# Performance work log

Hardware: AMD Instinct MI355X
Metric: run time of the kernel (lower is better)

## Reference

```python
import jax, jax.numpy as jnp
import numpy as np
import math

DIM = 256
PATCH = 16  # Patchnum
H = W = 64  # feature_size
B = 16


def _conv(x, w, pad):
    # x: [B,C,H,W], w: [O,I,kh,kw]
    return jax.lax.conv_general_dilated(
        x, w, window_strides=(1, 1), padding=[(pad, pad), (pad, pad)],
        dimension_numbers=('NCHW', 'OIHW', 'NCHW'))


def setup_inputs() -> dict:
    key = jax.random.key(0)
    ks = jax.random.split(key, 6)
    fan = DIM * 9
    s3 = 1.0 / math.sqrt(fan)
    s1 = 1.0 / math.sqrt(DIM)
    return {
        'e': jax.random.normal(ks[0], (B, DIM, H, W), dtype=jnp.float32),
        'pam_out': jax.random.normal(ks[1], (B, DIM, PATCH, PATCH), dtype=jnp.float32),
        'q_w': jax.random.uniform(ks[2], (DIM, DIM, 3, 3), jnp.float32, -s3, s3),
        'k_w': jax.random.uniform(ks[3], (DIM, DIM, 3, 3), jnp.float32, -s3, s3),
        'v_w': jax.random.uniform(ks[4], (DIM, DIM, 3, 3), jnp.float32, -s3, s3),
        'proj_w': jax.random.uniform(ks[5], (DIM, DIM, 1, 1), jnp.float32, -s1, s1),
    }


def reference(e, pam_out, q_w, k_w, v_w, proj_w):
    b, c, h, w = e.shape
    # AdaptiveAvgPool2d((PATCH, PATCH)) with h % PATCH == 0 -> mean pooling
    fh, fw = h // PATCH, w // PATCH
    max_e = e.reshape(b, c, PATCH, fh, PATCH, fw).mean(axis=(3, 5))
    q = _conv(max_e, q_w, 1).reshape(b, c, PATCH * PATCH)      # [b,c,P^2]
    k = _conv(pam_out, k_w, 1).reshape(b, c, PATCH * PATCH)    # [b,c,P^2]
    v = _conv(e, v_w, 1).reshape(b, c, h * w)                  # [b,c,HW]
    # L2 normalize along token dim (torch F.normalize, eps=1e-12)
    q = q / jnp.maximum(jnp.linalg.norm(q, axis=-1, keepdims=True), 1e-12)
    k = k / jnp.maximum(jnp.linalg.norm(k, axis=-1, keepdims=True), 1e-12)
    attn = jnp.einsum('bcn,bdn->bcd', q, k) / math.sqrt(c)     # [b,c,c]
    attn = jax.nn.softmax(attn, axis=-1)
    out = jnp.einsum('bcd,bdn->bcn', attn, v).reshape(b, c, h, w)
    out = _conv(out, proj_w, 0) + e
    return out
```

## Files before the change

### kernel.cpp

```cpp
#include <hip/hip_runtime.h>
#include <hip/hip_bf16.h>

#define NB 16
#define NC 256
#define NPIX 4096

typedef __attribute__((ext_vector_type(8))) short short8;
typedef __attribute__((ext_vector_type(4))) short short4v;
typedef __attribute__((ext_vector_type(4))) float f32x4;

static __device__ __forceinline__ ushort f2bf(float f) {
    __hip_bfloat16 h = __float2bfloat16(f);
    return *(ushort*)&h;
}

static __device__ __forceinline__ void gload_lds16(const ushort* g, ushort* l) {
    __builtin_amdgcn_global_load_lds(
        (const __attribute__((address_space(1))) unsigned int*)g,
        (__attribute__((address_space(3))) unsigned int*)l, 16, 0, 0);
}

__global__ void __launch_bounds__(256) prep_k(
    const float* __restrict__ e, const float* __restrict__ pam,
    const float* __restrict__ qw, const float* __restrict__ kw,
    const float* __restrict__ vw, const float* __restrict__ pw,
    ushort* __restrict__ et, ushort* __restrict__ maxeT, ushort* __restrict__ pamT,
    ushort* __restrict__ wqT, ushort* __restrict__ wkT,
    ushort* __restrict__ pbf, ushort* __restrict__ vwT,
    float* __restrict__ qnorm, float* __restrict__ knorm) {
    __shared__ float smem[9216];
    int blk = blockIdx.x, t = threadIdx.x;
    if (blk < 512) {
        int b = blk >> 5;
        int py = (blk >> 1) & 15;
        int xh = blk & 1;
        float (*lt)[32] = (float(*)[32])smem;
        float pool[8];
#pragma unroll
        for (int rr = 0; rr < 8; ++rr) pool[rr] = 0.f;
        int px = t & 7;
        int x4 = px * 4;
        int cg = t >> 3;
        for (int r = 0; r < 4; ++r) {
            int y = py * 4 + r;
            if (r) __syncthreads();
            const float* ep = e + (size_t)b * NC * NPIX + y * 64 + xh * 32;
#pragma unroll
            for (int rr = 0; rr < 8; ++rr) {
                int c = rr * 32 + cg;
                float4 v = *(const float4*)(ep + (size_t)c * NPIX + x4);
                pool[rr] += v.x + v.y + v.z + v.w;
                int s = (c >> 3) & 31;
                lt[c][(x4 + 0) ^ s] = v.x;
                lt[c][(x4 + 1) ^ s] = v.y;
                lt[c][(x4 + 2) ^ s] = v.z;
                lt[c][(x4 + 3) ^ s] = v.w;
            }
            __syncthreads();
            int l = t & 31, c0 = l * 8;
            ushort* op = et + ((size_t)((b * 64 + y) * 64) + xh * 32) * 256;
#pragma unroll
            for (int rx = 0; rx < 4; ++rx) {
                int x = rx * 8 + (t >> 5);
                short8 v;
#pragma unroll
                for (int k = 0; k < 8; ++k) v[k] = (short)f2bf(lt[c0 + k][x ^ l]);
                *(short8*)(op + (size_t)x * 256 + c0) = v;
            }
        }
        int tok = py * 16 + xh * 8 + px;
        ushort* md = maxeT + (size_t)b * 65536 + (size_t)tok * 256;
#pragma unroll
        for (int rr = 0; rr < 8; ++rr)
            md[rr * 32 + cg] = f2bf(pool[rr] * 0.0625f);
    } else if (blk < 768) {
        int bb = blk - 512;
        int b = bb >> 4, cg = bb & 15;
        float (*lt)[256] = (float(*)[256])smem;
#pragma unroll
        for (int cc = 0; cc < 16; ++cc)
            lt[cc][t] = pam[(size_t)(b * 256 + cg * 16 + cc) * 256 + t];
        __syncthreads();
        ushort* dstb = pamT + (size_t)b * 65536 + (size_t)t * 256 + cg * 16;
#pragma unroll
        for (int g = 0; g < 2; ++g) {
            short8 v;
#pragma unroll
            for (int k = 0; k < 8; ++k) v[k] = (short)f2bf(lt[g * 8 + k][t]);
            *(short8*)(dstb + g * 8) = v;
        }
    } else if (blk < 1280) {
        int idx = blk - 768;
        const float* src = (idx < 256) ? qw : kw;
        ushort* dst = (idx < 256) ? wqT : wkT;
        int o = idx & 255;
        float wv[9];
#pragma unroll
        for (int j = 0; j < 9; ++j) wv[j] = src[(size_t)o * 2304 + t * 9 + j];
#pragma unroll
        for (int j = 0; j < 9; ++j) dst[(size_t)j * 65536 + (size_t)o * 256 + t] = f2bf(wv[j]);
    } else if (blk < 1296) {
        int base = (blk - 1280) * 4096;
        for (int g = 0; g < 16; ++g) {
            int idx = base + g * 256 + t;
            pbf[idx] = f2bf(pw[idx]);
        }
    } else if (blk < 1360) {
        int d0 = (blk - 1296) * 4;
        float* lt = smem;
        for (int u = 0; u < 36; ++u) lt[u * 256 + t] = vw[(size_t)d0 * 2304 + u * 256 + t];
        __syncthreads();
#pragma unroll
        for (int r = 0; r < 9; ++r) {
            int idx = r * 256 + t;
            int i = idx / 9, j = idx % 9;
            short4v v;
#pragma unroll
            for (int dd = 0; dd < 4; ++dd) v[dd] = (short)f2bf(lt[dd * 2304 + idx]);
            *(short4v*)(vwT + ((size_t)(j * 256 + i)) * 256 + d0) = v;
        }
    } else {
        for (int g = 0; g < 16; ++g) {
            qnorm[g * 256 + t] = 0.f;
            knorm[g * 256 + t] = 0.f;
        }
    }
}

__global__ void __launch_bounds__(256, 2) conv16_mfma(const ushort* __restrict__ maxeT,
                                                      const ushort* __restrict__ pamT,
                                                      const ushort* __restrict__ wqT,
                                                      const ushort* __restrict__ wkT,
                                                      ushort* __restrict__ qb,
                                                      ushort* __restrict__ kTb,
                                                      float* __restrict__ qnorm,
                                                      float* __restrict__ knorm) {
    int blk = blockIdx.x;
    int qk = blk >> 8;
    int b  = (blk >> 4) & 15;
    int og = (blk >> 2) & 3;
    int tg = blk & 3;
    const ushort* inT = qk ? pamT : maxeT;
    const ushort* wt  = qk ? wkT : wqT;
    ushort* outp      = qk ? kTb : qb;
    float* nrm        = qk ? knorm : qnorm;
    int tid = threadIdx.x, wid = tid >> 6, lane = tid & 63;
    int wm = wid >> 1, wn = wid & 1;
    int kq = lane >> 4, l16 = lane & 15;
    int ty0 = tg * 4;
    __shared__ ushort Bs[96][256];
    __shared__ ushort As[2][64][128];
    const ushort* itb = inT + (size_t)b * 65536;
    {
#pragma unroll
        for (int j = 0; j < 12; ++j) {
            int d = (j * 4 + wid) * 64 + lane;
            int tok = d >> 5, u = d & 31;
            int lr = tok >> 4, tx = tok & 15;
            int gy = min(max(ty0 - 1 + lr, 0), 15);
            gload_lds16(itb + (gy * 16 + tx) * 256 + ((u ^ (tok & 7)) * 8),
                        &Bs[0][0] + (size_t)(j * 4 + wid) * 512);
        }
    }
    int aoff[4];
#pragma unroll
    for (int j = 0; j < 4; ++j) {
        int d = (j * 4 + wid) * 64 + lane;
        int o = d >> 4, u = d & 15;
        aoff[j] = (og * 64 + o) * 256 + ((u ^ (o & 7)) * 8);
    }
    auto stageA = [&](int s, int buf) {
        const ushort* base = wt + (size_t)(s >> 1) * 65536 + (s & 1) * 128;
#pragma unroll
        for (int j = 0; j < 4; ++j)
            gload_lds16(base + aoff[j], &As[buf][0][0] + (size_t)(j * 4 + wid) * 512);
    };
    stageA(0, 0);
    stageA(1, 1);
    __syncthreads();
    f32x4 acc[2][2];
#pragma unroll
    for (int mf = 0; mf < 2; ++mf)
#pragma unroll
        for (int nf = 0; nf < 2; ++nf) acc[mf][nf] = (f32x4){0.f, 0.f, 0.f, 0.f};
    const short8 zf = {};
#pragma unroll
    for (int s = 0; s < 18; ++s) {
        int tap = s >> 1, half = s & 1;
        int dy = tap / 3 - 1, dx = tap % 3 - 1;
        const ushort* bp[2]; bool ok[2]; int lt7[2];
#pragma unroll
        for (int nf = 0; nf < 2; ++nf) {
            int n = tg * 64 + wn * 32 + nf * 16 + l16;
            int ny = (n >> 4) + dy, nx = (n & 15) + dx;
            ok[nf] = ((unsigned)ny < 16u) && ((unsigned)nx < 16u);
            int lrc = min(max(ny - ty0 + 1, 0), 5);
            int nxc = min(max(nx, 0), 15);
            int ltok = lrc * 16 + nxc;
            bp[nf] = &Bs[ltok][0];
            lt7[nf] = ltok & 7;
        }
#pragma unroll
        for (int kc = 0; kc < 4; ++kc) {
            int ua = kc * 4 + kq;
            int ub = half * 16 + kc * 4 + kq;
            short8 af[2], bfr[2];
#pragma unroll
            for (int mf = 0; mf < 2; ++mf) {
                int o = wm * 32 + mf * 16 + l16;
                af[mf] = *(const short8*)(&As[s & 1][o][(ua ^ (o & 7)) * 8]);
            }
#pragma unroll
            for (int nf = 0; nf < 2; ++nf) {
                short8 v = *(const short8*)(bp[nf] + ((ub ^ lt7[nf]) * 8));
                bfr[nf] = ok[nf] ? v : zf;
            }
#pragma unroll
            for (int mf = 0; mf < 2; ++mf)
#pragma unroll
                for (int nf = 0; nf < 2; ++nf)
                    acc[mf][nf] = __builtin_amdgcn_mfma_f32_16x16x32_bf16(af[mf], bfr[nf], acc[mf][nf], 0, 0, 0);
        }
        __syncthreads();
        if (s + 2 < 18) stageA(s + 2, s & 1);
    }
    float ss[2][4];
#pragma unroll
    for (int mf = 0; mf < 2; ++mf)
#pragma unroll
        for (int r = 0; r < 4; ++r) ss[mf][r] = 0.f;
#pragma unroll
    for (int mf = 0; mf < 2; ++mf)
#pragma unroll
        for (int nf = 0; nf < 2; ++nf)
#pragma unroll
            for (int r = 0; r < 4; ++r) ss[mf][r] += acc[mf][nf][r] * acc[mf][nf][r];
#pragma unroll
    for (int mf = 0; mf < 2; ++mf)
#pragma unroll
        for (int r = 0; r < 4; ++r) {
#pragma unroll
            for (int off = 1; off < 16; off <<= 1) ss[mf][r] += __shfl_xor(ss[mf][r], off, 64);
        }
    if (l16 == 0) {
#pragma unroll
        for (int mf = 0; mf < 2; ++mf)
#pragma unroll
            for (int r = 0; r < 4; ++r)
                atomicAdd(&nrm[b * 256 + og * 64 + wm * 32 + mf * 16 + kq * 4 + r], ss[mf][r]);
    }
    ushort* ob = outp + (size_t)b * 65536;
#pragma unroll
    for (int mf = 0; mf < 2; ++mf)
#pragma unroll
        for (int nf = 0; nf < 2; ++nf) {
            int col = tg * 64 + wn * 32 + nf * 16 + l16;
#pragma unroll
            for (int r = 0; r < 4; ++r) {
                int row = og * 64 + wm * 32 + mf * 16 + kq * 4 + r;
                ob[(size_t)row * 256 + col] = f2bf(acc[mf][nf][r]);
            }
        }
}

__global__ void __launch_bounds__(512) attn_mfma(const ushort* __restrict__ qb,
                                                 const ushort* __restrict__ kTb,
                                                 const float* __restrict__ qnorm,
                                                 const float* __restrict__ knorm,
                                                 ushort* __restrict__ attnT) {
    int blk = blockIdx.x;
    int b = (blk & 7) + 8 * ((blk >> 3) & 1);
    int cg = blk >> 4;
    int tid = threadIdx.x, wid = tid >> 6, lane = tid & 63;
    int rw = wid & 1, chf = wid >> 1;
    int kq = lane >> 4, l16 = lane & 15;
    int c0w = cg * 32 + rw * 16;
    int lrow = rw * 16 + kq * 4;
    f32x4 acc[4];
#pragma unroll
    for (int nf = 0; nf < 4; ++nf) acc[nf] = (f32x4){0.f, 0.f, 0.f, 0.f};
    const ushort* qp = qb + (size_t)b * 65536;
    const ushort* kp = kTb + (size_t)b * 65536 + (size_t)(chf * 64) * 256;
    for (int kc = 0; kc < 8; ++kc) {
        short8 af = *(const short8*)(qp + (size_t)(c0w + l16) * 256 + kc * 32 + kq * 8);
#pragma unroll
        for (int nf = 0; nf < 4; ++nf) {
            short8 bf = *(const short8*)(kp + (size_t)(nf * 16 + l16) * 256 + kc * 32 + kq * 8);
            acc[nf] = __builtin_amdgcn_mfma_f32_16x16x32_bf16(af, bf, acc[nf], 0, 0, 0);
        }
    }
    float rq[4], rk[4];
#pragma unroll
    for (int r = 0; r < 4; ++r)
        rq[r] = rsqrtf(fmaxf(qnorm[b * 256 + c0w + kq * 4 + r], 1e-24f)) * 0.0625f;
#pragma unroll
    for (int nf = 0; nf < 4; ++nf)
        rk[nf] = rsqrtf(fmaxf(knorm[b * 256 + chf * 64 + nf * 16 + l16], 1e-24f));
#pragma unroll
    for (int nf = 0; nf < 4; ++nf)
#pragma unroll
        for (int r = 0; r < 4; ++r) acc[nf][r] *= rq[r] * rk[nf];
    __shared__ float red[32][4];
    float m4[4], s4[4];
#pragma unroll
    for (int r = 0; r < 4; ++r) {
        float m = -1e30f;
#pragma unroll
        for (int nf = 0; nf < 4; ++nf) m = fmaxf(m, acc[nf][r]);
#pragma unroll
        for (int off = 1; off < 16; off <<= 1) m = fmaxf(m, __shfl_xor(m, off, 64));
        m4[r] = m;
    }
    if (l16 == 0) {
#pragma unroll
        for (int r = 0; r < 4; ++r) red[lrow + r][chf] = m4[r];
    }
    __syncthreads();
#pragma unroll
    for (int r = 0; r < 4; ++r)
        m4[r] = fmaxf(fmaxf(red[lrow + r][0], red[lrow + r][1]),
                      fmaxf(red[lrow + r][2], red[lrow + r][3]));
    __syncthreads();
#pragma unroll
    for (int r = 0; r < 4; ++r) {
        float s = 0.f;
#pragma unroll
        for (int nf = 0; nf < 4; ++nf) {
            float ex = __expf(acc[nf][r] - m4[r]);
            acc[nf][r] = ex;
            s += ex;
        }
#pragma unroll
        for (int off = 1; off < 16; off <<= 1) s += __shfl_xor(s, off, 64);
        s4[r] = s;
    }
    if (l16 == 0) {
#pragma unroll
        for (int r = 0; r < 4; ++r) red[lrow + r][chf] = s4[r];
    }
    __syncthreads();
#pragma unroll
    for (int r = 0; r < 4; ++r) {
        float inv = 1.0f / (red[lrow + r][0] + red[lrow + r][1] +
                            red[lrow + r][2] + red[lrow + r][3]);
#pragma unroll
        for (int nf = 0; nf < 4; ++nf) acc[nf][r] *= inv;
    }
    ushort* ap = attnT + (size_t)b * 65536;
#pragma unroll
    for (int nf = 0; nf < 4; ++nf) {
        int d = chf * 64 + nf * 16 + l16;
        short4v v;
#pragma unroll
        for (int r = 0; r < 4; ++r) v[r] = (short)f2bf(acc[nf][r]);
        *(short4v*)(ap + (size_t)d * 256 + c0w + kq * 4) = v;
    }
}

__global__ void __launch_bounds__(512) mproj_mfma(const ushort* __restrict__ pbf,
                                                  const ushort* __restrict__ attnT,
                                                  ushort* __restrict__ Mbf) {
    int blk = blockIdx.x;
    int b = (blk & 7) + 8 * ((blk >> 3) & 1);
    int og = blk >> 4;
    int tid = threadIdx.x, wid = tid >> 6, lane = tid & 63;
    int rw = wid & 1, chf = wid >> 1;
    int kq = lane >> 4, l16 = lane & 15;
    int o0w = og * 32 + rw * 16;
    f32x4 acc[4];
#pragma unroll
    for (int nf = 0; nf < 4; ++nf) acc[nf] = (f32x4){0.f, 0.f, 0.f, 0.f};
    const ushort* ap = attnT + (size_t)b * 65536 + (size_t)(chf * 64) * 256;
    for (int kc = 0; kc < 8; ++kc) {
        short8 af = *(const short8*)(pbf + (size_t)(o0w + l16) * 256 + kc * 32 + kq * 8);
#pragma unroll
        for (int nf = 0; nf < 4; ++nf) {
            short8 bf = *(const short8*)(ap + (size_t)(nf * 16 + l16) * 256 + kc * 32 + kq * 8);
            acc[nf] = __builtin_amdgcn_mfma_f32_16x16x32_bf16(af, bf, acc[nf], 0, 0, 0);
        }
    }
    ushort* mb = Mbf + (size_t)b * 65536;
#pragma unroll
    for (int nf = 0; nf < 4; ++nf)
#pragma unroll
        for (int r = 0; r < 4; ++r)
            mb[(size_t)(o0w + kq * 4 + r) * 256 + chf * 64 + nf * 16 + l16] = f2bf(acc[nf][r]);
}

__global__ void __launch_bounds__(512) weff_mfma(const ushort* __restrict__ Mbf,
                                                 const ushort* __restrict__ vwT,
                                                 ushort* __restrict__ wbf) {
    int blk = blockIdx.x;
    int wg = (blk % 8) * 18 + blk / 8;
    int b = wg / 9, j = wg % 9;
    int tid = threadIdx.x;
    int wid = tid >> 6, lane = tid & 63;
    int wm = wid >> 1, wn = wid & 1;
    int kq = lane >> 4, l16 = lane & 15;
    f32x4 acc[4][8];
#pragma unroll
    for (int mf = 0; mf < 4; ++mf)
#pragma unroll
        for (int nf = 0; nf < 8; ++nf) acc[mf][nf] = (f32x4){0.f, 0.f, 0.f, 0.f};
    const ushort* abase = Mbf + (size_t)b * 65536 + (size_t)(wm * 64 + l16) * 256 + kq * 8;
    const ushort* bbase = vwT + (size_t)(j * 256 + wn * 128 + l16) * 256 + kq * 8;
    for (int kc = 0; kc < 8; ++kc) {
        int d0 = kc * 32;
        short8 af[4], bfr[8];
#pragma unroll
        for (int mf = 0; mf < 4; ++mf) af[mf] = *(const short8*)(abase + mf * 16 * 256 + d0);
#pragma unroll
        for (int nf = 0; nf < 8; ++nf) bfr[nf] = *(const short8*)(bbase + nf * 16 * 256 + d0);
#pragma unroll
        for (int mf = 0; mf < 4; ++mf)
#pragma unroll
            for (int nf = 0; nf < 8; ++nf)
                acc[mf][nf] = __builtin_amdgcn_mfma_f32_16x16x32_bf16(af[mf], bfr[nf], acc[mf][nf], 0, 0, 0);
    }
    ushort* wout = wbf + ((size_t)(b * 9 + j)) * 65536;
#pragma unroll
    for (int mf = 0; mf < 4; ++mf) {
        int o = wm * 64 + mf * 16 + kq * 4;
#pragma unroll
        for (int nf = 0; nf < 8; ++nf) {
            int ic = wn * 128 + nf * 16 + l16;
#pragma unroll
            for (int r = 0; r < 4; ++r)
                wout[(size_t)(o + r) * 256 + ic] = f2bf(acc[mf][nf][r]);
        }
    }
}

__global__ void __launch_bounds__(512, 4) bigconv_mfma(const ushort* __restrict__ et,
                                                       const ushort* __restrict__ wbf,
                                                       const float* __restrict__ e,
                                                       float* __restrict__ out) {
    int blk = blockIdx.x;
    int ibf = blk >> 3;
    int b = (blk & 7) + 8 * (ibf >> 5);
    int rem = ibf & 31;
    int pt = rem >> 1, oh = rem & 1;
    int y0 = pt * 4;
    int tid = threadIdx.x, wid = tid >> 6, lane = tid & 63;
    int wr = wid >> 1, wo = wid & 1;
    int kq = lane >> 4, l16 = lane & 15;
    __shared__ ushort Bs[6][64][32];
    __shared__ ushort As[3][128][32];
    f32x4 acc[4][4];
#pragma unroll
    for (int mf = 0; mf < 4; ++mf)
#pragma unroll
        for (int nf = 0; nf < 4; ++nf) acc[mf][nf] = (f32x4){0.f, 0.f, 0.f, 0.f};
    const ushort* etb = et + (size_t)b * 1048576;
    const float* eb = e + (size_t)b * NC * NPIX;
    const ushort* wb = wbf + (size_t)b * 589824;
    const short8 zf = {};
    int boff[3];
#pragma unroll
    for (int j = 0; j < 3; ++j) {
        int idx = j * 512 + tid;
        int row = idx >> 8;
        int px = (idx >> 2) & 63;
        int u = idx & 3;
        int yc = min(max(y0 - 1 + row, 0), 63);
        boff[j] = ((yc * 64 + px) << 8) + ((u ^ ((px >> 1) & 3)) * 8);
    }
    int ao_;
    {
        int o = tid >> 2, u = tid & 3;
        ao_ = (oh * 128 + o) * 256 + ((u ^ ((o >> 1) & 3)) * 8);
    }
    auto stageA = [&](int tap, int buf, int ci) {
        gload_lds16(wb + (size_t)tap * 65536 + ci * 32 + ao_,
                    &As[buf][0][0] + (size_t)tid * 8);
    };

    for (int ci = 0; ci < 8; ++ci) {
#pragma unroll
        for (int j = 0; j < 3; ++j)
            gload_lds16(etb + boff[j] + ci * 32,
                        &Bs[0][0][0] + (size_t)(j * 512 + tid) * 8);
        stageA(0, 0, ci);
        stageA(1, 1, ci);
        asm volatile("s_waitcnt vmcnt(1)" ::: "memory");
        __builtin_amdgcn_sched_barrier(0);
        __builtin_amdgcn_s_barrier();
#pragma unroll
        for (int tap = 0; tap < 9; ++tap) {
            int cur = tap % 3;
            {
                const int dy = tap / 3 - 1, dx = tap % 3 - 1;
                const int rl = wr + dy + 1;
                const bool rowok = (unsigned)(y0 + wr + dy) < 64u;
                const ushort* bp[4]; bool ok[4]; int p3[4];
#pragma unroll
                for (int nf = 0; nf < 4; ++nf) {
                    int pxr = nf * 16 + l16 + dx;
                    ok[nf] = rowok && ((unsigned)pxr < 64u);
                    int pxc = min(max(pxr, 0), 63);
                    bp[nf] = &Bs[rl][pxc][0];
                    p3[nf] = (pxc >> 1) & 3;
                }
                short8 af[4];
#pragma unroll
                for (int mf = 0; mf < 4; ++mf) {
                    int o = wo * 64 + mf * 16 + l16;
                    af[mf] = *(const short8*)(&As[cur][o][(kq ^ ((o >> 1) & 3)) * 8]);
                }
                short8 bfr[4];
#pragma unroll
                for (int nf = 0; nf < 4; ++nf) {
                    short8 v = *(const short8*)(bp[nf] + ((kq ^ p3[nf]) * 8));
                    bfr[nf] = ok[nf] ? v : zf;
                }
                __builtin_amdgcn_s_setprio(1);
#pragma unroll
                for (int mf = 0; mf < 4; ++mf)
#pragma unroll
                    for (int nf = 0; nf < 4; ++nf)
                        acc[mf][nf] = __builtin_amdgcn_mfma_f32_16x16x32_bf16(af[mf], bfr[nf], acc[mf][nf], 0, 0, 0);
                __builtin_amdgcn_s_setprio(0);
            }
            if (tap + 2 < 9) stageA(tap + 2, (tap + 2) % 3, ci);
            if (tap < 7) {
                asm volatile("s_waitcnt vmcnt(1)" ::: "memory");
            } else {
                asm volatile("s_waitcnt vmcnt(0)" ::: "memory");
            }
            __builtin_amdgcn_sched_barrier(0);
            __builtin_amdgcn_s_barrier();
        }
    }
    int prow = y0 + wr;
    float* ob = out + (size_t)b * NC * NPIX;
#pragma unroll
    for (int mf = 0; mf < 4; ++mf) {
        int o = oh * 128 + wo * 64 + mf * 16 + kq * 4;
#pragma unroll
        for (int nf = 0; nf < 4; ++nf) {
            int p = prow * 64 + nf * 16 + l16;
#pragma unroll
            for (int r = 0; r < 4; ++r) {
                size_t idx = (size_t)(o + r) * NPIX + p;
                ob[idx] = acc[mf][nf][r] + eb[idx];
            }
        }
    }
}

extern "C" void kernel_launch(void* const* d_in, const int* in_sizes, int n_in,
                              void* d_out, int out_size, void* d_ws, size_t ws_size,
                              hipStream_t stream) {
    const float* e   = (const float*)d_in[0];
    const float* pam = (const float*)d_in[1];
    const float* qw  = (const float*)d_in[2];
    const float* kw  = (const float*)d_in[3];
    const float* vw  = (const float*)d_in[4];
    const float* pw  = (const float*)d_in[5];
    float* out = (float*)d_out;
    float* ws  = (float*)d_ws;

    ushort* et   = (ushort*)ws;
    ushort* wbf  = (ushort*)(ws + 8388608);
    float*  S    = ws + 13107200;
    ushort* maxeT = (ushort*)S;
    ushort* pamT  = (ushort*)(S + 524288);
    ushort* wqT   = (ushort*)(S + 1048576);
    ushort* wkT   = (ushort*)(S + 1343488);
    ushort* pbf   = (ushort*)(S + 1638400);
    ushort* vwT   = (ushort*)(S + 1671168);
    float*  qnorm = S + 1966080;
    float*  knorm = S + 1970176;
    ushort* qb    = (ushort*)(ws + 8388608);
    ushort* kTb   = (ushort*)(ws + 8912896);
    ushort* attnT = maxeT;
    ushort* Mbf   = pamT;

    prep_k<<<1361, 256, 0, stream>>>(e, pam, qw, kw, vw, pw,
                                     et, maxeT, pamT, wqT, wkT, pbf, vwT, qnorm, knorm);
    conv16_mfma<<<512, 256, 0, stream>>>(maxeT, pamT, wqT, wkT, qb, kTb, qnorm, knorm);
    attn_mfma<<<128, 512, 0, stream>>>(qb, kTb, qnorm, knorm, attnT);
    mproj_mfma<<<128, 512, 0, stream>>>(pbf, attnT, Mbf);
    weff_mfma<<<144, 512, 0, stream>>>(Mbf, vwT, wbf);
    bigconv_mfma<<<512, 512, 0, stream>>>(et, wbf, e, out);
}
```

Measured before the change: 173.9 us.

## Double-buffer B tile across input-channel chunks in the output conv

Adds a second LDS buffer for the activation (B) tile and prefetches the next channel chunk's B and first two weight taps during the last taps of the current chunk. This removes the exposed load stall and barrier at the start of each of the 8 channel-chunk iterations. The cost is doubled B shared memory (48KB B plus 24KB A), which may reduce occupancy below the 4-blocks launch bound.

```diff
diff --git a/kernel.cpp b/kernel.cpp
--- a/kernel.cpp
+++ b/kernel.cpp
@@ -444,7 +444,7 @@
     int tid = threadIdx.x, wid = tid >> 6, lane = tid & 63;
     int wr = wid >> 1, wo = wid & 1;
     int kq = lane >> 4, l16 = lane & 15;
-    __shared__ ushort Bs[6][64][32];
+    __shared__ ushort Bs[2][6][64][32];
     __shared__ ushort As[3][128][32];
     f32x4 acc[4][4];
 #pragma unroll
@@ -474,20 +474,24 @@
         gload_lds16(wb + (size_t)tap * 65536 + ci * 32 + ao_,
                     &As[buf][0][0] + (size_t)tid * 8);
     };
-
-    for (int ci = 0; ci < 8; ++ci) {
+    auto stageB = [&](int ci, int buf) {
 #pragma unroll
         for (int j = 0; j < 3; ++j)
             gload_lds16(etb + boff[j] + ci * 32,
-                        &Bs[0][0][0] + (size_t)(j * 512 + tid) * 8);
-        stageA(0, 0, ci);
-        stageA(1, 1, ci);
-        asm volatile("s_waitcnt vmcnt(1)" ::: "memory");
-        __builtin_amdgcn_sched_barrier(0);
-        __builtin_amdgcn_s_barrier();
+                        &Bs[buf][0][0][0] + (size_t)(j * 512 + tid) * 8);
+    };
+
+    stageB(0, 0);
+    stageA(0, 0, 0);
+    stageA(1, 1, 0);
+    asm volatile("s_waitcnt vmcnt(1)" ::: "memory");
+    __builtin_amdgcn_sched_barrier(0);
+    __builtin_amdgcn_s_barrier();
+
+    for (int ci = 0; ci < 8; ++ci) {
+        int cb = ci & 1;
 #pragma unroll
         for (int tap = 0; tap < 9; ++tap) {
-            int cur = tap % 3;
             {
                 const int dy = tap / 3 - 1, dx = tap % 3 - 1;
                 const int rl = wr + dy + 1;
@@ -498,14 +502,14 @@
                     int pxr = nf * 16 + l16 + dx;
                     ok[nf] = rowok && ((unsigned)pxr < 64u);
                     int pxc = min(max(pxr, 0), 63);
-                    bp[nf] = &Bs[rl][pxc][0];
+                    bp[nf] = &Bs[cb][rl][pxc][0];
                     p3[nf] = (pxc >> 1) & 3;
                 }
                 short8 af[4];
 #pragma unroll
                 for (int mf = 0; mf < 4; ++mf) {
                     int o = wo * 64 + mf * 16 + l16;
-                    af[mf] = *(const short8*)(&As[cur][o][(kq ^ ((o >> 1) & 3)) * 8]);
+                    af[mf] = *(const short8*)(&As[tap % 3][o][(kq ^ ((o >> 1) & 3)) * 8]);
                 }
                 short8 bfr[4];
 #pragma unroll
@@ -521,11 +525,24 @@
                         acc[mf][nf] = __builtin_amdgcn_mfma_f32_16x16x32_bf16(af[mf], bfr[nf], acc[mf][nf], 0, 0, 0);
                 __builtin_amdgcn_s_setprio(0);
             }
-            if (tap + 2 < 9) stageA(tap + 2, (tap + 2) % 3, ci);
-            if (tap < 7) {
+            if (tap <= 6) {
+                stageA(tap + 2, (tap + 2) % 3, ci);
                 asm volatile("s_waitcnt vmcnt(1)" ::: "memory");
+            } else if (tap == 7) {
+                if (ci < 7) {
+                    stageB(ci + 1, cb ^ 1);
+                    asm volatile("s_waitcnt vmcnt(3)" ::: "memory");
+                } else {
+                    asm volatile("s_waitcnt vmcnt(0)" ::: "memory");
+                }
             } else {
-                asm volatile("s_waitcnt vmcnt(0)" ::: "memory");
+                if (ci < 7) {
+                    stageA(0, 0, ci + 1);
+                    stageA(1, 1, ci + 1);
+                    asm volatile("s_waitcnt vmcnt(1)" ::: "memory");
+                } else {
+                    asm volatile("s_waitcnt vmcnt(0)" ::: "memory");
+                }
             }
             __builtin_amdgcn_sched_barrier(0);
             __builtin_amdgcn_s_barrier();
```

After: 175.1 us. No clear change (+0.7%).
